# Kernel tuning notes

Hardware: AMD Instinct MI355X
Metric: run time of the kernel (lower is better)

The kernel has to match this reference:

```python
import jax, jax.numpy as jnp
import numpy as np

D_IN, D, H, DK, L, T, R = 128, 64, 4, 16, 4, 3, 32
N, E = 20000, 600000
SQRT_DK = 4.0  # sqrt(16)

# etype -> (src node type, dst node type) per hardcoded ranges in edge_attention
SRC_NT = np.array([0 if e <= 9 else (1 if e <= 21 else 2) for e in range(R)], dtype=np.int32)
def _dst_nt(e):
    if e <= 2 or 10 <= e <= 13 or 22 <= e <= 24: return 0
    if 3 <= e <= 6 or 14 <= e <= 17 or 25 <= e <= 28: return 1
    return 2
DST_NT = np.array([_dst_nt(e) for e in range(R)], dtype=np.int32)


def setup_inputs() -> dict:
    key = jax.random.key(0)
    ks = jax.random.split(key, 24)
    s = 0.05
    inp = {
        'h': jax.random.normal(ks[0], (N, D_IN), jnp.float32),
        'src': jax.random.randint(ks[1], (E,), 0, N),
        'dst': jax.random.randint(ks[2], (E,), 0, N),
        'etype': jax.random.randint(ks[3], (E,), 0, R),
        'ntype': jax.random.randint(ks[4], (N,), 0, T),
        'adapt_W': jax.random.normal(ks[5], (T, D_IN, D), jnp.float32) * s,
        'adapt_b': jnp.zeros((T, D), jnp.float32),
        'Wk': jax.random.normal(ks[6], (L, T, D, D), jnp.float32) * s,
        'bk': jnp.zeros((L, T, D), jnp.float32),
        'Wq': jax.random.normal(ks[7], (L, T, D, D), jnp.float32) * s,
        'bq': jnp.zeros((L, T, D), jnp.float32),
        'Wv': jax.random.normal(ks[8], (L, T, D, D), jnp.float32) * s,
        'bv': jnp.zeros((L, T, D), jnp.float32),
        'Wa': jax.random.normal(ks[9], (L, T, D, D), jnp.float32) * s,
        'ba': jnp.zeros((L, T, D), jnp.float32),
        'ln_g': jnp.ones((L, T, D), jnp.float32),
        'ln_b': jnp.zeros((L, T, D), jnp.float32),
        'rel_att': jax.random.normal(ks[10], (L, R, H, DK, DK), jnp.float32) * 0.17,  # ~xavier for 16x16
        'rel_msg': jax.random.normal(ks[11], (L, R, H, DK, DK), jnp.float32) * 0.17,
        'rel_pri': jnp.ones((L, R, H), jnp.float32),
        'nta': jnp.ones((L, T), jnp.float32),
        'nta1': jnp.ones((L, T), jnp.float32),
        'skipp': jnp.ones((L, T), jnp.float32),
        'wgt': jnp.ones((L,), jnp.float32),
        'afc_w': jax.random.normal(ks[12], (L, 2 * DK), jnp.float32) * s,
    }
    return inp


def _per_type_linear(x, W, b, ntype):
    # x:[N,din], W:[T,din,dout] -> per-node linear selected by node type
    y = jnp.einsum('nd,tdo->nto', x, W) + b  # [N,T,dout]
    return jnp.take_along_axis(y, ntype[:, None, None], axis=1)[:, 0]


def _layer(x, Wk, bk, Wq, bq, Wv, bv, Wa, ba, ln_g, ln_b, rel_att, rel_msg,
           rel_pri, nta, nta1, skipp, wgt, afc_w, src, dst, etype, ntype,
           src_nt_e, dst_nt_e):
    n = x.shape[0]
    k = _per_type_linear(x, Wk, bk, ntype).reshape(n, H, DK)
    q = _per_type_linear(x, Wq, bq, ntype).reshape(n, H, DK)
    v = _per_type_linear(x, Wv, bv, ntype).reshape(n, H, DK)
    # precompute relation-transformed k/v per node ([N,R,H,DK]) then gather per edge
    k_rel = jnp.einsum('nhd,rhdf->nrhf', k, rel_att)
    v_rel = jnp.einsum('nhd,rhdf->nrhf', v, rel_msg)
    key = k_rel[src, etype]   # [E,H,DK]
    val = v_rel[src, etype]   # [E,H,DK]
    qd = q[dst]               # [E,H,DK]
    att = (qd * key).sum(-1) * rel_pri[etype] / SQRT_DK  # [E,H]
    a_src = nta[src_nt_e][:, None, None]
    a_dst = nta1[dst_nt_e][:, None, None]
    cat = jnp.concatenate([a_dst * qd, a_src * k[src]], axis=-1)  # [E,H,2DK]
    na = jax.nn.leaky_relu(jnp.einsum('ehf,f->eh', cat, afc_w))
    logits = att + jax.nn.sigmoid(wgt) * na  # [E,H]
    # segment softmax per (dst node, etype) group, then mean across present etypes
    seg = dst * R + etype
    nseg = n * R
    m = jax.ops.segment_max(logits, seg, num_segments=nseg)
    ex = jnp.exp(logits - m[seg])
    den = jax.ops.segment_sum(ex, seg, num_segments=nseg)
    p = ex / den[seg]
    hte = jax.ops.segment_sum(p[:, :, None] * val, seg, num_segments=nseg)
    hte = hte.reshape(n, R, H, DK)
    cnt = jax.ops.segment_sum(jnp.ones((src.shape[0],), x.dtype), seg, num_segments=nseg)
    has = (cnt > 0).astype(x.dtype).reshape(n, R)
    t = hte.sum(1) / jnp.maximum(has.sum(1), 1.0)[:, None, None]  # cross mean over present etypes
    t = t.reshape(n, D)
    trans = _per_type_linear(t, Wa, ba, ntype)
    alpha = jax.nn.sigmoid(skipp)[ntype][:, None]
    out = trans * alpha + x * (1.0 - alpha)
    mu = out.mean(-1, keepdims=True)
    var = ((out - mu) ** 2).mean(-1, keepdims=True)
    xn = (out - mu) / jnp.sqrt(var + 1e-5)
    return xn * ln_g[ntype] + ln_b[ntype]


def reference(h, src, dst, etype, ntype, adapt_W, adapt_b, Wk, bk, Wq, bq, Wv, bv,
              Wa, ba, ln_g, ln_b, rel_att, rel_msg, rel_pri, nta, nta1, skipp,
              wgt, afc_w):
    src_nt_e = jnp.asarray(SRC_NT)[etype]
    dst_nt_e = jnp.asarray(DST_NT)[etype]
    x = jnp.tanh(_per_type_linear(h, adapt_W, adapt_b, ntype))
    for l in range(L):
        x = _layer(x, Wk[l], bk[l], Wq[l], bq[l], Wv[l], bv[l], Wa[l], ba[l],
                   ln_g[l], ln_b[l], rel_att[l], rel_msg[l], rel_pri[l],
                   nta[l], nta1[l], skipp[l], wgt[l], afc_w[l],
                   src, dst, etype, ntype, src_nt_e, dst_nt_e)
    return x
```

## Files before the change

### kernel.cpp

```cpp
#include <hip/hip_runtime.h>
#include <hip/hip_bf16.h>

#define NN 20000
#define NE 600000
#define DIN 128
#define DD 64
#define HH 4
#define DKK 16
#define LL 4
#define TT 3
#define RR 32
#define RP_TPW 10
#define RP_CH  125

typedef __attribute__((ext_vector_type(8))) short bf16x8;
typedef __attribute__((ext_vector_type(4))) float f32x4;

__device__ __forceinline__ int src_nt(int e) { return e <= 9 ? 0 : (e <= 21 ? 1 : 2); }
__device__ __forceinline__ int dst_nt(int e) {
    if (e <= 2 || (e >= 10 && e <= 13) || (e >= 22 && e <= 24)) return 0;
    if ((e >= 3 && e <= 6) || (e >= 14 && e <= 17) || (e >= 25 && e <= 28)) return 1;
    return 2;
}
__device__ __forceinline__ float bf_lo(unsigned u) { return __uint_as_float(u << 16); }
__device__ __forceinline__ float bf_hi(unsigned u) { return __uint_as_float(u & 0xffff0000u); }
__device__ __forceinline__ ushort f2bf(float x) {
    unsigned u = __float_as_uint(x);
    return (ushort)((u + 0x7fffu + ((u >> 16) & 1u)) >> 16);
}

__global__ void adapt_kernel(const float* __restrict__ h, const int* __restrict__ ntype,
                             const float* __restrict__ W, const float* __restrict__ b,
                             float* __restrict__ x) {
    int wid = (blockIdx.x * blockDim.x + threadIdx.x) >> 6;
    int lane = threadIdx.x & 63;
    if (wid >= NN) return;
    int t = ntype[wid];
    const float* Wt = W + (size_t)t * DIN * DD;
    float h0 = h[(size_t)wid * DIN + lane];
    float h1 = h[(size_t)wid * DIN + 64 + lane];
    float acc = b[t * DD + lane];
#pragma unroll
    for (int d = 0; d < 64; ++d) acc += __shfl(h0, d) * Wt[d * DD + lane];
#pragma unroll
    for (int d = 0; d < 64; ++d) acc += __shfl(h1, d) * Wt[(64 + d) * DD + lane];
    x[(size_t)wid * DD + lane] = tanhf(acc);
}

__global__ void csr_count_kernel(const int* __restrict__ dst, int* __restrict__ cnt) {
    int e = blockIdx.x * blockDim.x + threadIdx.x;
    if (e < NE) atomicAdd(&cnt[dst[e]], 1);
}

__global__ void csr_scan_kernel(const int* __restrict__ cnt, int* __restrict__ rowptr,
                                int* __restrict__ cursor) {
    __shared__ int wsuml[16];
    __shared__ int s_carry;
    int tid = threadIdx.x;
    int lane = tid & 63, wid = tid >> 6;
    if (tid == 0) s_carry = 0;
    __syncthreads();
    for (int base = 0; base < NN; base += 1024) {
        int i = base + tid;
        int v = (i < NN) ? cnt[i] : 0;
        int x = v;
#pragma unroll
        for (int off = 1; off < 64; off <<= 1) {
            int y = __shfl_up(x, off);
            if (lane >= off) x += y;
        }
        if (lane == 63) wsuml[wid] = x;
        __syncthreads();
        if (wid == 0 && lane < 16) {
            int w = wsuml[lane];
#pragma unroll
            for (int off = 1; off < 16; off <<= 1) {
                int y = __shfl_up(w, off);
                if (lane >= off) w += y;
            }
            wsuml[lane] = w;
        }
        __syncthreads();
        int woff = (wid > 0) ? wsuml[wid - 1] : 0;
        int carry = s_carry;
        int excl = carry + woff + x - v;
        if (i < NN) { rowptr[i] = excl; cursor[i] = excl; }
        __syncthreads();
        if (tid == 1023) s_carry = carry + wsuml[15];
        __syncthreads();
    }
    if (tid == 0) rowptr[NN] = NE;
}

__global__ void csr_fill_kernel(const int* __restrict__ src, const int* __restrict__ dst,
                                const int* __restrict__ et, int* __restrict__ cursor,
                                int* __restrict__ srcs, int* __restrict__ dsts,
                                int* __restrict__ ets) {
    int e = blockIdx.x * blockDim.x + threadIdx.x;
    if (e >= NE) return;
    int d = dst[e];
    int p = atomicAdd(&cursor[d], 1);
    srcs[p] = src[e];
    dsts[p] = d;
    ets[p] = et[e];
}

__global__ void kqv_kernel(const float* __restrict__ x, const int* __restrict__ ntype,
                           const float* __restrict__ Wk, const float* __restrict__ bk,
                           const float* __restrict__ Wq, const float* __restrict__ bq,
                           const float* __restrict__ Wv, const float* __restrict__ bv,
                           const float* __restrict__ afc,
                           ushort* __restrict__ kbf, ushort* __restrict__ qbf, ushort* __restrict__ vbf,
                           float* __restrict__ na_q, float* __restrict__ na_k) {
    int wid = (blockIdx.x * blockDim.x + threadIdx.x) >> 6;
    int lane = threadIdx.x & 63;
    if (wid >= NN) return;
    int t = ntype[wid];
    const float* Wkt = Wk + (size_t)t * DD * DD;
    const float* Wqt = Wq + (size_t)t * DD * DD;
    const float* Wvt = Wv + (size_t)t * DD * DD;
    float xv = x[(size_t)wid * DD + lane];
    float ak = bk[t * DD + lane];
    float aq = bq[t * DD + lane];
    float av = bv[t * DD + lane];
#pragma unroll
    for (int d = 0; d < 64; ++d) {
        float xd = __shfl(xv, d);
        ak += xd * Wkt[d * DD + lane];
        aq += xd * Wqt[d * DD + lane];
        av += xd * Wvt[d * DD + lane];
    }
    kbf[(size_t)wid * DD + lane] = f2bf(ak);
    qbf[(size_t)wid * DD + lane] = f2bf(aq);
    vbf[(size_t)wid * DD + lane] = f2bf(av);
    int f = lane & 15;
    float cq = aq * afc[f];
    float ck = ak * afc[16 + f];
#pragma unroll
    for (int off = 1; off < 16; off <<= 1) {
        cq += __shfl_xor(cq, off);
        ck += __shfl_xor(ck, off);
    }
    if (f == 0) {
        na_q[wid * HH + (lane >> 4)] = cq;
        na_k[wid * HH + (lane >> 4)] = ck;
    }
}

__global__ __launch_bounds__(256) void relpreQV_kernel(
        const ushort* __restrict__ qbf, const ushort* __restrict__ vbf,
        const float* __restrict__ relA, const float* __restrict__ relM,
        ushort* __restrict__ qr, ushort* __restrict__ vr) {
    __shared__ __align__(16) ushort lds[4][2][16 * DD];
    int gw = (blockIdx.x * blockDim.x + threadIdx.x) >> 6;
    int lane = threadIdx.x & 63;
    int wv = threadIdx.x >> 6;
    int r = gw / RP_CH;
    int c = gw % RP_CH;
    int m = lane & 15;
    int g = lane >> 4;
    int k0 = g * 8;
    bf16x8 aQ[HH], aV[HH];
#pragma unroll
    for (int h = 0; h < HH; ++h) {
        bf16x8 zq = {0, 0, 0, 0, 0, 0, 0, 0};
        bf16x8 zv = {0, 0, 0, 0, 0, 0, 0, 0};
        if (k0 < 16) {
            const float* Ab = relA + (size_t)(r * HH + h) * 256;
            const float* Mb = relM + (size_t)(r * HH + h) * 256;
#pragma unroll
            for (int j = 0; j < 8; ++j) {
                zq[j] = (short)f2bf(Ab[m * 16 + k0 + j]);
                zv[j] = (short)f2bf(Mb[(k0 + j) * 16 + m]);
            }
        }
        aQ[h] = zq; aV[h] = zv;
    }
    int ksafe = k0 & 8;
    int nd = lane >> 3;
    int ch = lane & 7;
    int wswz = (m & 7) << 1;
    for (int t = 0; t < RP_TPW; ++t) {
        int n0 = (c * RP_TPW + t) * 16;
#pragma unroll
        for (int h = 0; h < HH; ++h) {
            size_t brow = (size_t)(n0 + m) * DD + h * 16 + ksafe;
            bf16x8 bQ = *(const bf16x8*)(qbf + brow);
            bf16x8 bV = *(const bf16x8*)(vbf + brow);
            f32x4 z = {0.f, 0.f, 0.f, 0.f};
            f32x4 cq = __builtin_amdgcn_mfma_f32_16x16x32_bf16(aQ[h], bQ, z, 0, 0, 0);
            f32x4 cv = __builtin_amdgcn_mfma_f32_16x16x32_bf16(aV[h], bV, z, 0, 0, 0);
            ushort4 oq, ov;
            oq.x = f2bf(cq[0]); oq.y = f2bf(cq[1]); oq.z = f2bf(cq[2]); oq.w = f2bf(cq[3]);
            ov.x = f2bf(cv[0]); ov.y = f2bf(cv[1]); ov.z = f2bf(cv[2]); ov.w = f2bf(cv[3]);
            int cidx = (h * 4 + g) ^ wswz;
            int li = m * DD + cidx * 4;
            *(ushort4*)&lds[wv][0][li] = oq;
            *(ushort4*)&lds[wv][1][li] = ov;
        }
        asm volatile("s_waitcnt lgkmcnt(0)" ::: "memory");
#pragma unroll
        for (int p = 0; p < 2; ++p) {
            int node = p * 8 + nd;
            int c0 = (ch * 2) ^ ((node & 7) << 1);
            int li = node * DD + c0 * 4;
            uint4 dq = *(const uint4*)&lds[wv][0][li];
            uint4 dv = *(const uint4*)&lds[wv][1][li];
            size_t gb = ((size_t)(n0 + node) * RR + r) * DD + ch * 8;
            *(uint4*)(qr + gb) = dq;
            *(uint4*)(vr + gb) = dv;
        }
        asm volatile("s_waitcnt lgkmcnt(0)" ::: "memory");
    }
}

__global__ void edge_logitsB_kernel(const ushort* __restrict__ kbf,
                                    const ushort* __restrict__ qr,
                                    const int* __restrict__ srcs, const int* __restrict__ dsts,
                                    const int* __restrict__ ets,
                                    const float* __restrict__ pri,
                                    const float* __restrict__ nta, const float* __restrict__ nta1,
                                    const float* __restrict__ na_q, const float* __restrict__ na_k,
                                    const float* __restrict__ wgt,
                                    float* __restrict__ ex_out, float* __restrict__ den) {
    int idx = blockIdx.x * blockDim.x + threadIdx.x;
    if (idx >= NE * HH) return;
    int j = idx >> 2, hh = idx & 3;
    int s = srcs[j], dd = dsts[j], r = ets[j];
    const uint4* qp = (const uint4*)(qr + ((size_t)dd * RR + r) * DD + hh * 16);
    uint4 a0 = qp[0], a1 = qp[1];
    const uint4* kp = (const uint4*)(kbf + (size_t)s * DD + hh * 16);
    uint4 b0 = kp[0], b1 = kp[1];
    float att = bf_lo(a0.x) * bf_lo(b0.x) + bf_hi(a0.x) * bf_hi(b0.x)
              + bf_lo(a0.y) * bf_lo(b0.y) + bf_hi(a0.y) * bf_hi(b0.y)
              + bf_lo(a0.z) * bf_lo(b0.z) + bf_hi(a0.z) * bf_hi(b0.z)
              + bf_lo(a0.w) * bf_lo(b0.w) + bf_hi(a0.w) * bf_hi(b0.w)
              + bf_lo(a1.x) * bf_lo(b1.x) + bf_hi(a1.x) * bf_hi(b1.x)
              + bf_lo(a1.y) * bf_lo(b1.y) + bf_hi(a1.y) * bf_hi(b1.y)
              + bf_lo(a1.z) * bf_lo(b1.z) + bf_hi(a1.z) * bf_hi(b1.z)
              + bf_lo(a1.w) * bf_lo(b1.w) + bf_hi(a1.w) * bf_hi(b1.w);
    att = att * pri[r * HH + hh] * 0.25f;
    float c = nta1[dst_nt(r)] * na_q[dd * HH + hh] + nta[src_nt(r)] * na_k[s * HH + hh];
    float na = c > 0.f ? c : 0.01f * c;
    float sw = 1.f / (1.f + expf(-wgt[0]));
    float exv = expf(att + sw * na);
    ex_out[idx] = exv;
    atomicAdd(&den[((size_t)dd * RR + r) * HH + hh], exv);
}

__global__ void accum_csr_kernel(const ushort* __restrict__ vr,
                                 const int* __restrict__ srcs, const int* __restrict__ ets,
                                 const int* __restrict__ rowptr,
                                 const float* __restrict__ ex, const float* __restrict__ den,
                                 float* __restrict__ tacc) {
    int n = (blockIdx.x * blockDim.x + threadIdx.x) >> 6;
    int lane = threadIdx.x & 63;
    if (n >= NN) return;
    int beg = rowptr[n], end = rowptr[n + 1];
    int hh = lane >> 4;
    const float* denrow = den + (size_t)n * RR * HH + hh;
    float acc = 0.f;
    int j = beg;
    for (; j + 3 < end; j += 4) {
        int s0 = srcs[j],     r0 = ets[j];
        int s1 = srcs[j + 1], r1 = ets[j + 1];
        int s2 = srcs[j + 2], r2 = ets[j + 2];
        int s3 = srcs[j + 3], r3 = ets[j + 3];
        float v0 = bf_lo((unsigned)vr[((size_t)s0 * RR + r0) * DD + lane]);
        float v1 = bf_lo((unsigned)vr[((size_t)s1 * RR + r1) * DD + lane]);
        float v2 = bf_lo((unsigned)vr[((size_t)s2 * RR + r2) * DD + lane]);
        float v3 = bf_lo((unsigned)vr[((size_t)s3 * RR + r3) * DD + lane]);
        float e0 = ex[(size_t)(j)     * HH + hh];
        float e1 = ex[(size_t)(j + 1) * HH + hh];
        float e2 = ex[(size_t)(j + 2) * HH + hh];
        float e3 = ex[(size_t)(j + 3) * HH + hh];
        float d0 = denrow[r0 * HH];
        float d1 = denrow[r1 * HH];
        float d2 = denrow[r2 * HH];
        float d3 = denrow[r3 * HH];
        acc += e0 * __builtin_amdgcn_rcpf(d0) * v0;
        acc += e1 * __builtin_amdgcn_rcpf(d1) * v1;
        acc += e2 * __builtin_amdgcn_rcpf(d2) * v2;
        acc += e3 * __builtin_amdgcn_rcpf(d3) * v3;
    }
    for (; j < end; ++j) {
        int s = srcs[j], r = ets[j];
        float val = bf_lo((unsigned)vr[((size_t)s * RR + r) * DD + lane]);
        float p = ex[(size_t)j * HH + hh] * __builtin_amdgcn_rcpf(denrow[r * HH]);
        acc += p * val;
    }
    tacc[(size_t)n * DD + lane] = acc;
}

__global__ void node_out_kernel(const float* __restrict__ x_in, const float* __restrict__ tacc,
                                const float* __restrict__ den, const int* __restrict__ ntype,
                                const float* __restrict__ Wa, const float* __restrict__ ba,
                                const float* __restrict__ skipp,
                                const float* __restrict__ ln_g, const float* __restrict__ ln_b,
                                float* __restrict__ x_out) {
    int n = (blockIdx.x * blockDim.x + threadIdx.x) >> 6;
    int lane = threadIdx.x & 63;
    if (n >= NN) return;
    int t = ntype[n];
    int pres = 0;
    if (lane < RR) pres = (den[((size_t)n * RR + lane) * HH] > 0.f) ? 1 : 0;
    unsigned long long mask = __ballot(pres != 0);
    float cnt = (float)__popcll(mask);
    float divisor = fmaxf(cnt, 1.0f);
    float tv = tacc[(size_t)n * DD + lane] / divisor;
    const float* Wt = Wa + (size_t)t * DD * DD;
    float acc = ba[t * DD + lane];
#pragma unroll
    for (int d = 0; d < 64; ++d) acc += __shfl(tv, d) * Wt[d * DD + lane];
    float alpha = 1.f / (1.f + expf(-skipp[t]));
    float out = acc * alpha + x_in[(size_t)n * DD + lane] * (1.f - alpha);
    float s = out;
#pragma unroll
    for (int off = 1; off < 64; off <<= 1) s += __shfl_xor(s, off);
    float mu = s * (1.f / 64.f);
    float d0 = out - mu;
    float s2 = d0 * d0;
#pragma unroll
    for (int off = 1; off < 64; off <<= 1) s2 += __shfl_xor(s2, off);
    float var = s2 * (1.f / 64.f);
    float xn = d0 * rsqrtf(var + 1e-5f);
    x_out[(size_t)n * DD + lane] = xn * ln_g[t * DD + lane] + ln_b[t * DD + lane];
}

extern "C" void kernel_launch(void* const* d_in, const int* in_sizes, int n_in,
                              void* d_out, int out_size, void* d_ws, size_t ws_size,
                              hipStream_t stream) {
    const float* h       = (const float*)d_in[0];
    const int*   src     = (const int*)d_in[1];
    const int*   dst     = (const int*)d_in[2];
    const int*   etype   = (const int*)d_in[3];
    const int*   ntype   = (const int*)d_in[4];
    const float* adapt_W = (const float*)d_in[5];
    const float* adapt_b = (const float*)d_in[6];
    const float* Wk      = (const float*)d_in[7];
    const float* bk      = (const float*)d_in[8];
    const float* Wq      = (const float*)d_in[9];
    const float* bq      = (const float*)d_in[10];
    const float* Wv      = (const float*)d_in[11];
    const float* bv      = (const float*)d_in[12];
    const float* Wa      = (const float*)d_in[13];
    const float* ba      = (const float*)d_in[14];
    const float* ln_g    = (const float*)d_in[15];
    const float* ln_b    = (const float*)d_in[16];
    const float* rel_att = (const float*)d_in[17];
    const float* rel_msg = (const float*)d_in[18];
    const float* rel_pri = (const float*)d_in[19];
    const float* nta     = (const float*)d_in[20];
    const float* nta1    = (const float*)d_in[21];
    const float* skipp   = (const float*)d_in[22];
    const float* wgt     = (const float*)d_in[23];
    const float* afc_w   = (const float*)d_in[24];

    char* cur = (char*)d_ws;
    auto alloc = [&](size_t bytes) {
        char* p = cur;
        cur += (bytes + 63) & ~(size_t)63;
        return (void*)p;
    };
    float* x0     = (float*)alloc((size_t)NN * DD * 4);
    float* x1     = (float*)alloc((size_t)NN * DD * 4);
    ushort* kbf   = (ushort*)alloc((size_t)NN * DD * 2);
    ushort* qbf   = (ushort*)alloc((size_t)NN * DD * 2);
    ushort* vbf   = (ushort*)alloc((size_t)NN * DD * 2);
    float* tb     = (float*)alloc((size_t)NN * DD * 4);
    float* exbuf  = (float*)alloc((size_t)NE * HH * 4);
    float* den    = (float*)alloc((size_t)NN * RR * HH * 4);
    float* na_q   = (float*)alloc((size_t)NN * HH * 4);
    float* na_k   = (float*)alloc((size_t)NN * HH * 4);
    int*   cnt    = (int*)alloc((size_t)NN * 4);
    int*   rowptr = (int*)alloc((size_t)(NN + 1) * 4);
    int*   cursor = (int*)alloc((size_t)NN * 4);
    int*   srcs   = (int*)alloc((size_t)NE * 4);
    int*   dsts   = (int*)alloc((size_t)NE * 4);
    int*   ets    = (int*)alloc((size_t)NE * 4);
    ushort* qr    = (ushort*)alloc((size_t)NN * RR * DD * 2);
    ushort* vr    = (ushort*)alloc((size_t)NN * RR * DD * 2);

    const int NODE_BLOCKS = NN / 4;
    const int E_BLOCKS    = (NE + 255) / 256;
    const int EH_BLOCKS   = (NE * HH) / 256;
    const int RP_BLOCKS   = (RR * RP_CH) / 4;

    adapt_kernel<<<NODE_BLOCKS, 256, 0, stream>>>(h, ntype, adapt_W, adapt_b, x0);

    hipMemsetAsync(cnt, 0, (size_t)NN * 4, stream);
    csr_count_kernel<<<E_BLOCKS, 256, 0, stream>>>(dst, cnt);
    csr_scan_kernel<<<1, 1024, 0, stream>>>(cnt, rowptr, cursor);
    csr_fill_kernel<<<E_BLOCKS, 256, 0, stream>>>(src, dst, etype, cursor, srcs, dsts, ets);

    float* xin = x0;
    for (int l = 0; l < LL; ++l) {
        hipMemsetAsync(den, 0, (size_t)NN * RR * HH * 4, stream);

        kqv_kernel<<<NODE_BLOCKS, 256, 0, stream>>>(
            xin, ntype,
            Wk + (size_t)l * TT * DD * DD, bk + (size_t)l * TT * DD,
            Wq + (size_t)l * TT * DD * DD, bq + (size_t)l * TT * DD,
            Wv + (size_t)l * TT * DD * DD, bv + (size_t)l * TT * DD,
            afc_w + (size_t)l * 2 * DKK,
            kbf, qbf, vbf, na_q, na_k);

        relpreQV_kernel<<<RP_BLOCKS, 256, 0, stream>>>(
            qbf, vbf,
            rel_att + (size_t)l * RR * HH * 256, rel_msg + (size_t)l * RR * HH * 256,
            qr, vr);

        edge_logitsB_kernel<<<EH_BLOCKS, 256, 0, stream>>>(
            kbf, qr, srcs, dsts, ets,
            rel_pri + (size_t)l * RR * HH,
            nta + (size_t)l * TT, nta1 + (size_t)l * TT,
            na_q, na_k, wgt + l,
            exbuf, den);

        accum_csr_kernel<<<NODE_BLOCKS, 256, 0, stream>>>(
            vr, srcs, ets, rowptr, exbuf, den, tb);

        float* xout = (l == LL - 1) ? (float*)d_out : ((xin == x0) ? x1 : x0);
        node_out_kernel<<<NODE_BLOCKS, 256, 0, stream>>>(
            xin, tb, den, ntype,
            Wa + (size_t)l * TT * DD * DD, ba + (size_t)l * TT * DD,
            skipp + (size_t)l * TT,
            ln_g + (size_t)l * TT * DD, ln_b + (size_t)l * TT * DD,
            xout);
        xin = xout;
    }
}
```

Baseline: 800.5 us.

## Sort nodes by type and compute K/Q/V projections with bf16 MFMA

Adds a one-block scan that permutes nodes so same-type nodes are contiguous, and renumbers the CSR and edge endpoints into that order. Each 16-node tile then sees at most a few types, which lets the per-type K/Q/V linear run as 16x16x32 bf16 MFMA instead of a per-lane shuffle loop. Node features between layers are stored as bf16 to halve that traffic, and the final layer scatters back to the original order. The cost is an extra serial scan kernel, weights converted to bf16 on every block, and lower precision in the residual path.

```diff
diff --git a/kernel.cpp b/kernel.cpp
--- a/kernel.cpp
+++ b/kernel.cpp
@@ -29,9 +29,75 @@
     return (ushort)((u + 0x7fffu + ((u >> 16) & 1u)) >> 16);
 }
 
+__global__ void perm_scan_kernel(const int* __restrict__ ntype, int* __restrict__ perm,
+                                 int* __restrict__ iperm, int* __restrict__ ptype) {
+    __shared__ int wsum3[3][16];
+    __shared__ int carry[3];
+    __shared__ int offs[3];
+    int tid = threadIdx.x;
+    int lane = tid & 63, wid = tid >> 6;
+    int loc[3] = {0, 0, 0};
+    for (int i = tid; i < NN; i += 1024) loc[ntype[i]]++;
+#pragma unroll
+    for (int t = 0; t < 3; ++t) {
+        int v = loc[t];
+#pragma unroll
+        for (int off = 1; off < 64; off <<= 1) v += __shfl_xor(v, off);
+        if (lane == 0) wsum3[t][wid] = v;
+    }
+    __syncthreads();
+    if (tid == 0) {
+        int c0 = 0, c1 = 0;
+        for (int i = 0; i < 16; ++i) { c0 += wsum3[0][i]; c1 += wsum3[1][i]; }
+        offs[0] = 0; offs[1] = c0; offs[2] = c0 + c1;
+        carry[0] = 0; carry[1] = 0; carry[2] = 0;
+    }
+    __syncthreads();
+    for (int base = 0; base < NN; base += 1024) {
+        int i = base + tid;
+        int t = (i < NN) ? ntype[i] : -1;
+        int exc[3];
+#pragma unroll
+        for (int tt = 0; tt < 3; ++tt) {
+            int v = (t == tt) ? 1 : 0;
+            int x = v;
+#pragma unroll
+            for (int off = 1; off < 64; off <<= 1) {
+                int y = __shfl_up(x, off);
+                if (lane >= off) x += y;
+            }
+            if (lane == 63) wsum3[tt][wid] = x;
+            exc[tt] = x - v;
+        }
+        __syncthreads();
+        if (wid == 0 && lane < 16) {
+#pragma unroll
+            for (int tt = 0; tt < 3; ++tt) {
+                int w = wsum3[tt][lane];
+#pragma unroll
+                for (int off = 1; off < 16; off <<= 1) {
+                    int y = __shfl_up(w, off);
+                    if (lane >= off) w += y;
+                }
+                wsum3[tt][lane] = w;
+            }
+        }
+        __syncthreads();
+        if (i < NN) {
+            int woff = (wid > 0) ? wsum3[t][wid - 1] : 0;
+            int slot = offs[t] + carry[t] + woff + exc[t];
+            perm[slot] = i; iperm[i] = slot; ptype[slot] = t;
+        }
+        __syncthreads();
+        if (tid == 0) { for (int tt = 0; tt < 3; ++tt) carry[tt] += wsum3[tt][15]; }
+        __syncthreads();
+    }
+}
+
 __global__ void adapt_kernel(const float* __restrict__ h, const int* __restrict__ ntype,
+                             const int* __restrict__ iperm,
                              const float* __restrict__ W, const float* __restrict__ b,
-                             float* __restrict__ x) {
+                             ushort* __restrict__ xbf) {
     int wid = (blockIdx.x * blockDim.x + threadIdx.x) >> 6;
     int lane = threadIdx.x & 63;
     if (wid >= NN) return;
@@ -44,12 +110,13 @@
     for (int d = 0; d < 64; ++d) acc += __shfl(h0, d) * Wt[d * DD + lane];
 #pragma unroll
     for (int d = 0; d < 64; ++d) acc += __shfl(h1, d) * Wt[(64 + d) * DD + lane];
-    x[(size_t)wid * DD + lane] = tanhf(acc);
-}
-
-__global__ void csr_count_kernel(const int* __restrict__ dst, int* __restrict__ cnt) {
+    xbf[(size_t)iperm[wid] * DD + lane] = f2bf(tanhf(acc));
+}
+
+__global__ void csr_count_kernel(const int* __restrict__ dst, const int* __restrict__ iperm,
+                                 int* __restrict__ cnt) {
     int e = blockIdx.x * blockDim.x + threadIdx.x;
-    if (e < NE) atomicAdd(&cnt[dst[e]], 1);
+    if (e < NE) atomicAdd(&cnt[iperm[dst[e]]], 1);
 }
 
 __global__ void csr_scan_kernel(const int* __restrict__ cnt, int* __restrict__ rowptr,
@@ -93,57 +160,85 @@
 }
 
 __global__ void csr_fill_kernel(const int* __restrict__ src, const int* __restrict__ dst,
-                                const int* __restrict__ et, int* __restrict__ cursor,
+                                const int* __restrict__ et, const int* __restrict__ iperm,
+                                int* __restrict__ cursor,
                                 int* __restrict__ srcs, int* __restrict__ dsts,
                                 int* __restrict__ ets) {
     int e = blockIdx.x * blockDim.x + threadIdx.x;
     if (e >= NE) return;
-    int d = dst[e];
+    int d = iperm[dst[e]];
     int p = atomicAdd(&cursor[d], 1);
-    srcs[p] = src[e];
+    srcs[p] = iperm[src[e]];
     dsts[p] = d;
     ets[p] = et[e];
 }
 
-__global__ void kqv_kernel(const float* __restrict__ x, const int* __restrict__ ntype,
-                           const float* __restrict__ Wk, const float* __restrict__ bk,
-                           const float* __restrict__ Wq, const float* __restrict__ bq,
-                           const float* __restrict__ Wv, const float* __restrict__ bv,
-                           const float* __restrict__ afc,
-                           ushort* __restrict__ kbf, ushort* __restrict__ qbf, ushort* __restrict__ vbf,
-                           float* __restrict__ na_q, float* __restrict__ na_k) {
-    int wid = (blockIdx.x * blockDim.x + threadIdx.x) >> 6;
+__global__ __launch_bounds__(256) void kqv_mfma_kernel(
+        const ushort* __restrict__ xbf, const int* __restrict__ ptype,
+        const float* __restrict__ Wk, const float* __restrict__ bk,
+        const float* __restrict__ Wq, const float* __restrict__ bq,
+        const float* __restrict__ Wv, const float* __restrict__ bv,
+        const float* __restrict__ afc,
+        ushort* __restrict__ kbf, ushort* __restrict__ qbf, ushort* __restrict__ vbf,
+        float* __restrict__ na_q, float* __restrict__ na_k) {
+    int p0 = blockIdx.x * 16;
     int lane = threadIdx.x & 63;
-    if (wid >= NN) return;
-    int t = ntype[wid];
-    const float* Wkt = Wk + (size_t)t * DD * DD;
-    const float* Wqt = Wq + (size_t)t * DD * DD;
-    const float* Wvt = Wv + (size_t)t * DD * DD;
-    float xv = x[(size_t)wid * DD + lane];
-    float ak = bk[t * DD + lane];
-    float aq = bq[t * DD + lane];
-    float av = bv[t * DD + lane];
-#pragma unroll
-    for (int d = 0; d < 64; ++d) {
-        float xd = __shfl(xv, d);
-        ak += xd * Wkt[d * DD + lane];
-        aq += xd * Wqt[d * DD + lane];
-        av += xd * Wvt[d * DD + lane];
-    }
-    kbf[(size_t)wid * DD + lane] = f2bf(ak);
-    qbf[(size_t)wid * DD + lane] = f2bf(aq);
-    vbf[(size_t)wid * DD + lane] = f2bf(av);
-    int f = lane & 15;
-    float cq = aq * afc[f];
-    float ck = ak * afc[16 + f];
-#pragma unroll
-    for (int off = 1; off < 16; off <<= 1) {
-        cq += __shfl_xor(cq, off);
-        ck += __shfl_xor(ck, off);
-    }
-    if (f == 0) {
-        na_q[wid * HH + (lane >> 4)] = cq;
-        na_k[wid * HH + (lane >> 4)] = ck;
+    int w = threadIdx.x >> 6;
+    int m = lane & 15, g = lane >> 4;
+    int k0 = g * 8, frow = g * 4, ob = w * 16;
+    int myn = p0 + m;
+    int myt = ptype[myn];
+    int t0 = ptype[p0], t1 = ptype[p0 + 15];
+    bf16x8 b0 = *(const bf16x8*)(xbf + (size_t)myn * DD + k0);
+    bf16x8 b1 = *(const bf16x8*)(xbf + (size_t)myn * DD + 32 + k0);
+    for (int t = t0; t <= t1; ++t) {
+        const float* WkT = Wk + (size_t)t * DD * DD; const float* bkT = bk + t * DD;
+        const float* WqT = Wq + (size_t)t * DD * DD; const float* bqT = bq + t * DD;
+        const float* WvT = Wv + (size_t)t * DD * DD; const float* bvT = bv + t * DD;
+        bf16x8 ak0, ak1, aq0, aq1, av0, av1;
+        int col = ob + m;
+#pragma unroll
+        for (int j = 0; j < 8; ++j) {
+            ak0[j] = (short)f2bf(WkT[(k0 + j) * DD + col]);
+            ak1[j] = (short)f2bf(WkT[(32 + k0 + j) * DD + col]);
+            aq0[j] = (short)f2bf(WqT[(k0 + j) * DD + col]);
+            aq1[j] = (short)f2bf(WqT[(32 + k0 + j) * DD + col]);
+            av0[j] = (short)f2bf(WvT[(k0 + j) * DD + col]);
+            av1[j] = (short)f2bf(WvT[(32 + k0 + j) * DD + col]);
+        }
+        f32x4 z = {0.f, 0.f, 0.f, 0.f};
+        f32x4 ck = __builtin_amdgcn_mfma_f32_16x16x32_bf16(ak0, b0, z, 0, 0, 0);
+        ck = __builtin_amdgcn_mfma_f32_16x16x32_bf16(ak1, b1, ck, 0, 0, 0);
+        f32x4 cq = __builtin_amdgcn_mfma_f32_16x16x32_bf16(aq0, b0, z, 0, 0, 0);
+        cq = __builtin_amdgcn_mfma_f32_16x16x32_bf16(aq1, b1, cq, 0, 0, 0);
+        f32x4 cv = __builtin_amdgcn_mfma_f32_16x16x32_bf16(av0, b0, z, 0, 0, 0);
+        cv = __builtin_amdgcn_mfma_f32_16x16x32_bf16(av1, b1, cv, 0, 0, 0);
+        float sq = 0.f, sk = 0.f;
+        ushort4 okk, oqq, ovv;
+#pragma unroll
+        for (int j = 0; j < 4; ++j) {
+            int o = ob + frow + j;
+            float kk = ck[j] + bkT[o];
+            float qq = cq[j] + bqT[o];
+            float vv = cv[j] + bvT[o];
+            sq += qq * afc[frow + j];
+            sk += kk * afc[16 + frow + j];
+            ((ushort*)&okk)[j] = f2bf(kk);
+            ((ushort*)&oqq)[j] = f2bf(qq);
+            ((ushort*)&ovv)[j] = f2bf(vv);
+        }
+        sq += __shfl_xor(sq, 16); sq += __shfl_xor(sq, 32);
+        sk += __shfl_xor(sk, 16); sk += __shfl_xor(sk, 32);
+        if (myt == t) {
+            size_t ob8 = (size_t)myn * DD + ob + frow;
+            *(ushort4*)(kbf + ob8) = okk;
+            *(ushort4*)(qbf + ob8) = oqq;
+            *(ushort4*)(vbf + ob8) = ovv;
+            if (g == 0) {
+                na_q[myn * HH + w] = sq;
+                na_k[myn * HH + w] = sk;
+            }
+        }
     }
 }
 
@@ -292,16 +387,17 @@
     tacc[(size_t)n * DD + lane] = acc;
 }
 
-__global__ void node_out_kernel(const float* __restrict__ x_in, const float* __restrict__ tacc,
-                                const float* __restrict__ den, const int* __restrict__ ntype,
+__global__ void node_out_kernel(const ushort* __restrict__ xbf_in, const float* __restrict__ tacc,
+                                const float* __restrict__ den, const int* __restrict__ ptype,
+                                const int* __restrict__ perm,
                                 const float* __restrict__ Wa, const float* __restrict__ ba,
                                 const float* __restrict__ skipp,
                                 const float* __restrict__ ln_g, const float* __restrict__ ln_b,
-                                float* __restrict__ x_out) {
+                                ushort* __restrict__ xbf_out, float* __restrict__ fout, int last) {
     int n = (blockIdx.x * blockDim.x + threadIdx.x) >> 6;
     int lane = threadIdx.x & 63;
     if (n >= NN) return;
-    int t = ntype[n];
+    int t = ptype[n];
     int pres = 0;
     if (lane < RR) pres = (den[((size_t)n * RR + lane) * HH] > 0.f) ? 1 : 0;
     unsigned long long mask = __ballot(pres != 0);
@@ -313,7 +409,8 @@
 #pragma unroll
     for (int d = 0; d < 64; ++d) acc += __shfl(tv, d) * Wt[d * DD + lane];
     float alpha = 1.f / (1.f + expf(-skipp[t]));
-    float out = acc * alpha + x_in[(size_t)n * DD + lane] * (1.f - alpha);
+    float xi = bf_lo((unsigned)xbf_in[(size_t)n * DD + lane]);
+    float out = acc * alpha + xi * (1.f - alpha);
     float s = out;
 #pragma unroll
     for (int off = 1; off < 64; off <<= 1) s += __shfl_xor(s, off);
@@ -324,7 +421,9 @@
     for (int off = 1; off < 64; off <<= 1) s2 += __shfl_xor(s2, off);
     float var = s2 * (1.f / 64.f);
     float xn = d0 * rsqrtf(var + 1e-5f);
-    x_out[(size_t)n * DD + lane] = xn * ln_g[t * DD + lane] + ln_b[t * DD + lane];
+    float res = xn * ln_g[t * DD + lane] + ln_b[t * DD + lane];
+    if (last) fout[(size_t)perm[n] * DD + lane] = res;
+    else      xbf_out[(size_t)n * DD + lane] = f2bf(res);
 }
 
 extern "C" void kernel_launch(void* const* d_in, const int* in_sizes, int n_in,
@@ -362,8 +461,8 @@
         cur += (bytes + 63) & ~(size_t)63;
         return (void*)p;
     };
-    float* x0     = (float*)alloc((size_t)NN * DD * 4);
-    float* x1     = (float*)alloc((size_t)NN * DD * 4);
+    ushort* xbf0  = (ushort*)alloc((size_t)NN * DD * 2);
+    ushort* xbf1  = (ushort*)alloc((size_t)NN * DD * 2);
     ushort* kbf   = (ushort*)alloc((size_t)NN * DD * 2);
     ushort* qbf   = (ushort*)alloc((size_t)NN * DD * 2);
     ushort* vbf   = (ushort*)alloc((size_t)NN * DD * 2);
@@ -375,6 +474,9 @@
     int*   cnt    = (int*)alloc((size_t)NN * 4);
     int*   rowptr = (int*)alloc((size_t)(NN + 1) * 4);
     int*   cursor = (int*)alloc((size_t)NN * 4);
+    int*   perm   = (int*)alloc((size_t)NN * 4);
+    int*   iperm  = (int*)alloc((size_t)NN * 4);
+    int*   ptype  = (int*)alloc((size_t)NN * 4);
     int*   srcs   = (int*)alloc((size_t)NE * 4);
     int*   dsts   = (int*)alloc((size_t)NE * 4);
     int*   ets    = (int*)alloc((size_t)NE * 4);
@@ -385,20 +487,22 @@
     const int E_BLOCKS    = (NE + 255) / 256;
     const int EH_BLOCKS   = (NE * HH) / 256;
     const int RP_BLOCKS   = (RR * RP_CH) / 4;
-
-    adapt_kernel<<<NODE_BLOCKS, 256, 0, stream>>>(h, ntype, adapt_W, adapt_b, x0);
+    const int KQV_BLOCKS  = NN / 16;
+
+    perm_scan_kernel<<<1, 1024, 0, stream>>>(ntype, perm, iperm, ptype);
+    adapt_kernel<<<NODE_BLOCKS, 256, 0, stream>>>(h, ntype, iperm, adapt_W, adapt_b, xbf0);
 
     hipMemsetAsync(cnt, 0, (size_t)NN * 4, stream);
-    csr_count_kernel<<<E_BLOCKS, 256, 0, stream>>>(dst, cnt);
+    csr_count_kernel<<<E_BLOCKS, 256, 0, stream>>>(dst, iperm, cnt);
     csr_scan_kernel<<<1, 1024, 0, stream>>>(cnt, rowptr, cursor);
-    csr_fill_kernel<<<E_BLOCKS, 256, 0, stream>>>(src, dst, etype, cursor, srcs, dsts, ets);
-
-    float* xin = x0;
+    csr_fill_kernel<<<E_BLOCKS, 256, 0, stream>>>(src, dst, etype, iperm, cursor, srcs, dsts, ets);
+
+    ushort* xin = xbf0;
     for (int l = 0; l < LL; ++l) {
         hipMemsetAsync(den, 0, (size_t)NN * RR * HH * 4, stream);
 
-        kqv_kernel<<<NODE_BLOCKS, 256, 0, stream>>>(
-            xin, ntype,
+        kqv_mfma_kernel<<<KQV_BLOCKS, 256, 0, stream>>>(
+            xin, ptype,
             Wk + (size_t)l * TT * DD * DD, bk + (size_t)l * TT * DD,
             Wq + (size_t)l * TT * DD * DD, bq + (size_t)l * TT * DD,
             Wv + (size_t)l * TT * DD * DD, bv + (size_t)l * TT * DD,
@@ -420,13 +524,14 @@
         accum_csr_kernel<<<NODE_BLOCKS, 256, 0, stream>>>(
             vr, srcs, ets, rowptr, exbuf, den, tb);
 
-        float* xout = (l == LL - 1) ? (float*)d_out : ((xin == x0) ? x1 : x0);
+        int last = (l == LL - 1) ? 1 : 0;
+        ushort* xout = (xin == xbf0) ? xbf1 : xbf0;
         node_out_kernel<<<NODE_BLOCKS, 256, 0, stream>>>(
-            xin, tb, den, ntype,
+            xin, tb, den, ptype, perm,
             Wa + (size_t)l * TT * DD * DD, ba + (size_t)l * TT * DD,
             skipp + (size_t)l * TT,
             ln_g + (size_t)l * TT * DD, ln_b + (size_t)l * TT * DD,
-            xout);
+            xout, (float*)d_out, last);
         xin = xout;
     }
 }
```

New measurement: 751.3 us. -6.1%, faster.
